# Kernel optimization log

Measured on AMD Instinct MI355X. Metric: run time of the kernel, lower is better.

## Reference

```python
import jax, jax.numpy as jnp
import numpy as np

N, E, F, HID, OUT, B, HEADS = 4096, 131072, 64, 64, 86, 16, 4


def setup_inputs() -> dict:
    key = jax.random.key(0)
    ks = jax.random.split(key, 12)
    s = 0.1
    return {
        "x": jax.random.normal(ks[0], (N, F), dtype=jnp.float32),
        "edge_index": jax.random.randint(ks[1], (2, E), 0, N),
        "edge_attr": jax.random.uniform(ks[2], (E,), dtype=jnp.float32),
        "batch": jnp.sort(jax.random.randint(ks[3], (N,), 0, B)).astype(jnp.int32),
        # GCNConv1: Linear(F -> HID, no bias) + post-aggregation bias
        "W1": jax.random.normal(ks[4], (HID, F), dtype=jnp.float32) * s,
        "b1": jnp.zeros((HID,), jnp.float32),
        # MultiheadAttention(embed_dim=HID, num_heads=4)
        "Win": jax.random.normal(ks[5], (3 * HID, HID), dtype=jnp.float32) * s,
        "b_in": jnp.zeros((3 * HID,), jnp.float32),
        "Wout": jax.random.normal(ks[6], (HID, HID), dtype=jnp.float32) * s,
        "b_out": jnp.zeros((HID,), jnp.float32),
        # GCNConv2: Linear(HID -> OUT)
        "W2": jax.random.normal(ks[7], (OUT, HID), dtype=jnp.float32) * s,
        "b2": jnp.zeros((OUT,), jnp.float32),
    }


def _gcn_layer(h, W, b, src_a, dst_a, norm, n):
    # x' = scatter_add(norm * (x W^T)[src] -> dst) + b   (PyG GCNConv)
    h = h @ W.T
    agg = jax.ops.segment_sum(norm[:, None] * h[src_a], dst_a, num_segments=n)
    return agg + b


def reference(x, edge_index, edge_attr, batch, W1, b1, Win, b_in, Wout, b_out, W2, b2):
    n = x.shape[0]
    # torch.cat([x[:, :-1], x[:, -1:].view(-1,1)], dim=1) == x (identity)
    src, dst = edge_index[0], edge_index[1]
    loop = jnp.arange(n)
    src_a = jnp.concatenate([src, loop])
    dst_a = jnp.concatenate([dst, loop])
    w_a = jnp.concatenate([edge_attr, jnp.ones((n,), x.dtype)])  # self-loops weight 1
    deg = jax.ops.segment_sum(w_a, dst_a, num_segments=n)
    dis = jnp.where(deg > 0, jax.lax.rsqrt(jnp.maximum(deg, 1e-12)), 0.0)
    norm = dis[src_a] * w_a * dis[dst_a]

    h = jax.nn.relu(_gcn_layer(x, W1, b1, src_a, dst_a, norm, n))  # [N, HID]

    # MultiheadAttention over the whole node set as one sequence (batch=1)
    qkv = h @ Win.T + b_in
    q, k, v = jnp.split(qkv, 3, axis=-1)
    dh = HID // HEADS
    to_heads = lambda t: t.reshape(n, HEADS, dh).transpose(1, 0, 2)  # [H, N, dh]
    q, k, v = to_heads(q), to_heads(k), to_heads(v)
    scores = jnp.einsum("hnd,hmd->hnm", q, k) * (1.0 / np.sqrt(dh))
    att = jax.nn.softmax(scores, axis=-1)
    o = jnp.einsum("hnm,hmd->hnd", att, v).transpose(1, 0, 2).reshape(n, HID)
    o = o @ Wout.T + b_out

    h2 = _gcn_layer(o, W2, b2, src_a, dst_a, norm, n)  # [N, OUT]

    # global_mean_pool over graph ids
    sums = jax.ops.segment_sum(h2, batch, num_segments=B)
    cnt = jax.ops.segment_sum(jnp.ones((n,), h2.dtype), batch, num_segments=B)
    return sums / jnp.maximum(cnt, 1.0)[:, None]
```

## Files before the change

### kernel.cpp

```cpp
#include <hip/hip_runtime.h>
#include <hip/hip_bf16.h>

constexpr int N = 4096, E = 131072, OUTF = 86, NB = 16, HEADS = 4, DH = 16;
constexpr int CAP = 128;
constexpr int NSPLIT = 4, KEYS = N / NSPLIT;
constexpr int PCKS = 8;

typedef __attribute__((ext_vector_type(8))) short short8;
typedef __attribute__((ext_vector_type(4))) float f32x4;

constexpr unsigned long long PK_MASK = (1ULL << 40) - 1;
constexpr float PK_SCALE = 1.0f / 16777216.0f;

constexpr size_t OFF_PCK   = 0;
constexpr size_t OFF_INV   = OFF_PCK + 16 * (size_t)N;
constexpr size_t OFF_BUFA  = OFF_INV + 16;
constexpr size_t OFF_QP    = OFF_BUFA + (size_t)N * 64;
constexpr size_t OFF_KP    = OFF_QP + (size_t)N * 32;
constexpr size_t OFF_VP    = OFF_KP + (size_t)N * 32;
constexpr size_t OFF_H2    = OFF_VP + (size_t)N * 32;
constexpr size_t OFF_EPAIR = OFF_H2 + (size_t)N * 86;
constexpr size_t OFF_NORMV = OFF_EPAIR + (size_t)2 * N * CAP;
constexpr size_t OFF_OPART = OFF_NORMV + (size_t)N * CAP;
constexpr size_t OFF_LPART = OFF_OPART + (size_t)HEADS * N * NSPLIT * 16;

__device__ inline unsigned short f2bf(float f) {
    unsigned u = __builtin_bit_cast(unsigned, f);
    u += 0x7FFFu + ((u >> 16) & 1u);
    return (unsigned short)(u >> 16);
}

__device__ inline unsigned pk2bf(float a, float b) {
    __hip_bfloat162 h2 = __float22bfloat162_rn(make_float2(a, b));
    union { __hip_bfloat162 h; unsigned u; } c;
    c.h = h2;
    return c.u;
}

__device__ inline float pk_deg(unsigned long long pk) {
    return (float)(pk & PK_MASK) * PK_SCALE;
}

__global__ __launch_bounds__(256) void d1_kernel(const float* __restrict__ x,
        const float* __restrict__ W1, const int* __restrict__ ei,
        const float* __restrict__ ea, const int* __restrict__ batch,
        const float* __restrict__ b2, float* __restrict__ ws, float* __restrict__ out) {
    __shared__ float4 Ws4[64 * 17];
    __shared__ float4 As4[16 * 17];
    __shared__ int bnd[NB + 1];
    int blk = blockIdx.x, tid = threadIdx.x;
    if (blk < 256) {
        float* bufA = ws + OFF_BUFA;
        for (int idx = tid; idx < 64 * 16; idx += 256)
            Ws4[(idx >> 4) * 17 + (idx & 15)] = ((const float4*)W1)[idx];
        {
            int r = tid >> 4, k4 = tid & 15;
            As4[r * 17 + k4] = ((const float4*)x)[(size_t)(blk * 16 + r) * 16 + k4];
        }
        __syncthreads();
        int r2 = tid & 7, cg = tid >> 3;
        float acc[2][2] = {};
#pragma unroll
        for (int k4 = 0; k4 < 16; ++k4) {
            float4 a0 = As4[r2 * 17 + k4], a1 = As4[(r2 + 8) * 17 + k4];
#pragma unroll
            for (int i = 0; i < 2; ++i) {
                float4 w = Ws4[(cg + 32 * i) * 17 + k4];
                acc[0][i] += a0.x * w.x + a0.y * w.y + a0.z * w.z + a0.w * w.w;
                acc[1][i] += a1.x * w.x + a1.y * w.y + a1.z * w.z + a1.w * w.w;
            }
        }
#pragma unroll
        for (int j = 0; j < 2; ++j)
#pragma unroll
            for (int i = 0; i < 2; ++i)
                bufA[(size_t)(blk * 16 + r2 + 8 * j) * 64 + cg + 32 * i] = acc[j][i];
    } else if (blk < 512) {
        unsigned long long* pck = (unsigned long long*)(ws + OFF_PCK);
        int2* epair = (int2*)(ws + OFF_EPAIR);
        int f = (blk - 256) * 256 + tid;
        int e0 = f, e1 = f + E / 2;
        int s0 = ei[e0], d0 = ei[E + e0];
        int s1 = ei[e1], d1 = ei[E + e1];
        float w0 = ea[e0], w1 = ea[e1];
        unsigned long long a0 = (1ULL << 40) + (unsigned long long)(unsigned)(w0 * 16777216.0f + 0.5f);
        unsigned long long a1 = (1ULL << 40) + (unsigned long long)(unsigned)(w1 * 16777216.0f + 0.5f);
        unsigned long long o0 = atomicAdd(&pck[(size_t)d0 * PCKS], a0);
        unsigned long long o1 = atomicAdd(&pck[(size_t)d1 * PCKS], a1);
        int p0 = (int)(o0 >> 40), p1 = (int)(o1 >> 40);
        if (p0 < CAP) epair[(size_t)d0 * CAP + p0] = make_int2(s0, __float_as_int(w0));
        if (p1 < CAP) epair[(size_t)d1 * CAP + p1] = make_int2(s1, __float_as_int(w1));
    } else {
        float* invcnt = ws + OFF_INV;
        if (tid <= NB) {
            int b = tid, lo = 0, hi = N;
            while (lo < hi) { int m = (lo + hi) >> 1; if (batch[m] < b) lo = m + 1; else hi = m; }
            bnd[tid] = lo;
        }
        __syncthreads();
        if (tid < NB) {
            int cnt = bnd[tid + 1] - bnd[tid];
            invcnt[tid] = cnt > 0 ? 1.0f / (float)cnt : 0.0f;
        }
        for (int idx = tid; idx < NB * OUTF; idx += 256) {
            int b = idx / OUTF;
            int cnt = bnd[b + 1] - bnd[b];
            out[idx] = cnt > 0 ? b2[idx - b * OUTF] : 0.0f;
        }
    }
}

__global__ __launch_bounds__(1024) void d23_kernel(const float* __restrict__ Win,
        const float* __restrict__ b1, const float* __restrict__ b_in,
        float* __restrict__ ws) {
    __shared__ float4 Ws4[16 * 200];
    __shared__ float  Af[16 * 68];

    const unsigned long long* pck = (const unsigned long long*)(ws + OFF_PCK);
    const int2*  epair = (const int2*)(ws + OFF_EPAIR);
    float*       normv = ws + OFF_NORMV;
    const float* bufA  = ws + OFF_BUFA;
    unsigned short* Qp = (unsigned short*)(ws + OFF_QP);
    unsigned short* Kp = (unsigned short*)(ws + OFF_KP);
    unsigned short* Vp = (unsigned short*)(ws + OFF_VP);

    const int tid = threadIdx.x, lane = tid & 63, wv = tid >> 6;
    for (int idx = tid; idx < 192 * 16; idx += 1024) {
        int c = idx >> 4, k4 = idx & 15;
        Ws4[k4 * 200 + c] = ((const float4*)Win)[idx];
    }

    const int node = blockIdx.x * 16 + wv;
    {
        const unsigned long long pkn = pck[(size_t)node * PCKS];
        const float di = rsqrtf(pk_deg(pkn) + 1.0f);
        float acc0 = (di * di) * bufA[(size_t)node * 64 + lane];
        float acc1 = 0.f, acc2 = 0.f, acc3 = 0.f;
        const int cnt = min((int)(pkn >> 40), CAP);
        const int2* pe = epair + (size_t)node * CAP;
        for (int base = 0; base < cnt; base += 64) {
            int rem = cnt - base;
            int   sl = 0;
            float nl = 0.f;
            if (lane < rem) {
                int2 e = pe[base + lane];
                sl = e.x;
                float w = __int_as_float(e.y);
                nl = rsqrtf(pk_deg(pck[(size_t)sl * PCKS]) + 1.0f) * w * di;
                normv[(size_t)node * CAP + base + lane] = nl;
            }
            int m = rem < 64 ? rem : 64;
            int j = 0;
            for (; j + 8 <= m; j += 8) {
                int   s0 = __shfl(sl, j),     s1 = __shfl(sl, j + 1);
                int   s2 = __shfl(sl, j + 2), s3 = __shfl(sl, j + 3);
                int   s4 = __shfl(sl, j + 4), s5 = __shfl(sl, j + 5);
                int   s6 = __shfl(sl, j + 6), s7 = __shfl(sl, j + 7);
                float n0 = __shfl(nl, j),     n1 = __shfl(nl, j + 1);
                float n2 = __shfl(nl, j + 2), n3 = __shfl(nl, j + 3);
                float n4 = __shfl(nl, j + 4), n5 = __shfl(nl, j + 5);
                float n6 = __shfl(nl, j + 6), n7 = __shfl(nl, j + 7);
                float v0 = bufA[(size_t)s0 * 64 + lane], v1 = bufA[(size_t)s1 * 64 + lane];
                float v2 = bufA[(size_t)s2 * 64 + lane], v3 = bufA[(size_t)s3 * 64 + lane];
                float v4 = bufA[(size_t)s4 * 64 + lane], v5 = bufA[(size_t)s5 * 64 + lane];
                float v6 = bufA[(size_t)s6 * 64 + lane], v7 = bufA[(size_t)s7 * 64 + lane];
                acc0 += n0 * v0; acc1 += n1 * v1; acc2 += n2 * v2; acc3 += n3 * v3;
                acc0 += n4 * v4; acc1 += n5 * v5; acc2 += n6 * v6; acc3 += n7 * v7;
            }
            for (; j + 4 <= m; j += 4) {
                int   s0 = __shfl(sl, j),     s1 = __shfl(sl, j + 1);
                int   s2 = __shfl(sl, j + 2), s3 = __shfl(sl, j + 3);
                float n0 = __shfl(nl, j),     n1 = __shfl(nl, j + 1);
                float n2 = __shfl(nl, j + 2), n3 = __shfl(nl, j + 3);
                acc0 += n0 * bufA[(size_t)s0 * 64 + lane];
                acc1 += n1 * bufA[(size_t)s1 * 64 + lane];
                acc2 += n2 * bufA[(size_t)s2 * 64 + lane];
                acc3 += n3 * bufA[(size_t)s3 * 64 + lane];
            }
            for (; j < m; ++j) {
                int   s0 = __shfl(sl, j);
                float n0 = __shfl(nl, j);
                acc0 += n0 * bufA[(size_t)s0 * 64 + lane];
            }
        }
        Af[wv * 68 + lane] = fmaxf((acc0 + acc1) + (acc2 + acc3) + b1[lane], 0.0f);
    }
    __syncthreads();

    {
        const float4* Af4 = (const float4*)Af;
        float acc[3];
#pragma unroll
        for (int i = 0; i < 3; ++i) acc[i] = b_in[lane + 64 * i];
#pragma unroll
        for (int k4 = 0; k4 < 16; ++k4) {
            float4 a = Af4[wv * 17 + k4];
#pragma unroll
            for (int i = 0; i < 3; ++i) {
                float4 w = Ws4[k4 * 200 + lane + 64 * i];
                acc[i] += a.x * w.x + a.y * w.y + a.z * w.z + a.w * w.w;
            }
        }
        const int row = node;
#pragma unroll
        for (int i = 0; i < 3; ++i) {
            int c = lane + 64 * i;
            float v = acc[i];
            if (c < 64) {
                int h = c >> 4, d = c & 15;
                Qp[((size_t)h * N + row) * 16 + d] = f2bf(v * 0.25f);
            } else if (c < 128) {
                int c2 = c - 64, h = c2 >> 4, d = c2 & 15;
                Kp[((size_t)h * N + row) * 16 + d] = f2bf(v);
            } else {
                int c2 = c - 128, h = c2 >> 4, d = c2 & 15;
                Vp[((size_t)h * 16 + d) * N + row] = f2bf(v);
            }
        }
    }
}

__global__ __launch_bounds__(256) void attn_kernel(const float* __restrict__ ws_c,
        float* __restrict__ ws) {
    __shared__ __align__(16) unsigned short Plds[4 * 640];

    const unsigned short* Qp = (const unsigned short*)(ws_c + OFF_QP);
    const unsigned short* Kp = (const unsigned short*)(ws_c + OFF_KP);
    const unsigned short* Vp = (const unsigned short*)(ws_c + OFF_VP);
    float* opart = ws + OFF_OPART;
    float* lpart = ws + OFF_LPART;

    const int h  = blockIdx.y;
    const int sp = blockIdx.z;
    const int k0 = sp * KEYS;
    const int tid = threadIdx.x;
    const int lane = tid & 63, wv = tid >> 6;
    const int q15 = lane & 15, quad = lane >> 4;

    const int qbase = blockIdx.x * 64 + wv * 16;
    short8 qf = {};
    if (quad < 2)
        qf = *(const short8*)&Qp[((size_t)h * N + qbase + q15) * 16 + quad * 8];

    f32x4 O = {0.f, 0.f, 0.f, 0.f};
    float l = 0.f;
    unsigned short* Pw = &Plds[wv * 640];
    const unsigned short* Kh = Kp + (size_t)h * N * 16;
    const unsigned short* Vh = Vp + ((size_t)h * 16 + q15) * N + k0;

#pragma unroll 2
    for (int ch = 0; ch < KEYS / 32; ++ch) {
#pragma unroll
        for (int t = 0; t < 2; ++t) {
            short8 kf = {};
            if (quad < 2)
                kf = *(const short8*)&Kh[(size_t)(k0 + ch * 32 + t * 16 + q15) * 16 + quad * 8];
            f32x4 zero = {0.f, 0.f, 0.f, 0.f};
            __builtin_amdgcn_s_setprio(1);
            f32x4 s = __builtin_amdgcn_mfma_f32_16x16x32_bf16(kf, qf, zero, 0, 0, 0);
            __builtin_amdgcn_s_setprio(0);
            float p0 = __expf(s[0]), p1 = __expf(s[1]), p2 = __expf(s[2]), p3 = __expf(s[3]);
            l += (p0 + p1) + (p2 + p3);
            uint2 pk;
            pk.x = pk2bf(p0, p1);
            pk.y = pk2bf(p2, p3);
            *(uint2*)&Pw[q15 * 40 + t * 16 + quad * 4] = pk;
        }
        asm volatile("s_waitcnt lgkmcnt(0)" ::: "memory");
        short8 pf = *(const short8*)&Pw[q15 * 40 + quad * 8];
        short8 vf = *(const short8*)&Vh[ch * 32 + quad * 8];
        __builtin_amdgcn_s_setprio(1);
        O = __builtin_amdgcn_mfma_f32_16x16x32_bf16(pf, vf, O, 0, 0, 0);
        __builtin_amdgcn_s_setprio(0);
    }

    l += __shfl_xor(l, 16);
    l += __shfl_xor(l, 32);
    if (lane < 16)
        lpart[((size_t)h * N + qbase + q15) * NSPLIT + sp] = l;
#pragma unroll
    for (int r = 0; r < 4; ++r) {
        int query = qbase + quad * 4 + r;
        opart[(((size_t)h * N + query) * NSPLIT + sp) * 16 + q15] = O[r];
    }
}

__global__ __launch_bounds__(256) void d4b_kernel(const float* __restrict__ Wout,
        const float* __restrict__ b_out, const float* __restrict__ W2,
        float* __restrict__ ws) {
    __shared__ float4 WoS[64 * 17];
    __shared__ float4 W2S[96 * 17];
    __shared__ float  o_sh[16 * 68];
    __shared__ float  Bf[16 * 68];

    const float* opart = ws + OFF_OPART;
    const float* lpart = ws + OFF_LPART;
    float* h2pre = ws + OFF_H2;

    const int tid = threadIdx.x, qbase = blockIdx.x * 16;
    for (int idx = tid; idx < 64 * 16; idx += 256)
        WoS[(idx >> 4) * 17 + (idx & 15)] = ((const float4*)Wout)[idx];
    for (int idx = tid; idx < 86 * 16; idx += 256)
        W2S[(idx >> 4) * 17 + (idx & 15)] = ((const float4*)W2)[idx];

    for (int idx = tid; idx < 16 * 64; idx += 256) {
        int r = idx >> 6, f = idx & 63;
        int h = f >> 4, d = f & 15;
        size_t base = ((size_t)h * N + qbase + r) * NSPLIT;
        float L = 0.f, acc = 0.f;
#pragma unroll
        for (int s = 0; s < NSPLIT; ++s) {
            L += lpart[base + s];
            acc += opart[(base + s) * 16 + d];
        }
        o_sh[r * 68 + f] = acc / L;
    }
    __syncthreads();
    {
        int r = tid & 15, c0 = tid >> 4;
        float4* o4 = (float4*)o_sh;
#pragma unroll
        for (int i = 0; i < 4; ++i) {
            int c = c0 + 16 * i;
            float acc = b_out[c];
#pragma unroll
            for (int k4 = 0; k4 < 16; ++k4) {
                float4 a = o4[r * 17 + k4];
                float4 w = WoS[c * 17 + k4];
                acc += a.x * w.x + a.y * w.y + a.z * w.z + a.w * w.w;
            }
            Bf[r * 68 + c] = acc;
        }
    }
    __syncthreads();
    {
        int r = tid & 15, c0 = tid >> 4;
        float4* B4 = (float4*)Bf;
#pragma unroll
        for (int i = 0; i < 6; ++i) {
            int c = c0 + 16 * i;
            if (c < OUTF) {
                float acc = 0.f;
#pragma unroll
                for (int k4 = 0; k4 < 16; ++k4) {
                    float4 a = B4[r * 17 + k4];
                    float4 w = W2S[c * 17 + k4];
                    acc += a.x * w.x + a.y * w.y + a.z * w.z + a.w * w.w;
                }
                h2pre[(size_t)(qbase + r) * OUTF + c] = acc;
            }
        }
    }
}

__global__ __launch_bounds__(1024) void d5_kernel(const int* __restrict__ batch,
        float* __restrict__ ws, float* __restrict__ out) {
    __shared__ float vec[16][88];
    __shared__ int   bix[16];

    const unsigned long long* pck = (const unsigned long long*)(ws + OFF_PCK);
    const int2*  epair = (const int2*)(ws + OFF_EPAIR);
    const float* normv = ws + OFF_NORMV;
    const float* invcnt= ws + OFF_INV;
    const float* h2pre = ws + OFF_H2;

    const int tid = threadIdx.x;
    const int lane = tid & 63, wv = tid >> 6;
    const int node = blockIdx.x * 16 + wv;
    const bool hi2 = lane < (OUTF - 64);
    const int b = batch[node];
    const float inv = invcnt[b];
    const unsigned long long pkn = pck[(size_t)node * PCKS];
    const float di2 = 1.0f / (pk_deg(pkn) + 1.0f);
    const float* Hn = h2pre + (size_t)node * OUTF;
    float a0 = di2 * Hn[lane],                  a1 = 0.f, a2 = 0.f, a3 = 0.f;
    float c0 = hi2 ? di2 * Hn[64 + lane] : 0.f, c1 = 0.f, c2 = 0.f, c3 = 0.f;
    const int cnt = min((int)(pkn >> 40), CAP);
    const int2* pe = epair + (size_t)node * CAP;

    for (int base = 0; base < cnt; base += 64) {
        int rem = cnt - base;
        int   sl = 0;
        float nl = 0.f;
        if (lane < rem) {
            sl = pe[base + lane].x;
            nl = normv[(size_t)node * CAP + base + lane];
        }
        int m = rem < 64 ? rem : 64;
        int j = 0;
        for (; j + 8 <= m; j += 8) {
            int   s0 = __shfl(sl, j),     s1 = __shfl(sl, j + 1);
            int   s2 = __shfl(sl, j + 2), s3 = __shfl(sl, j + 3);
            int   s4 = __shfl(sl, j + 4), s5 = __shfl(sl, j + 5);
            int   s6 = __shfl(sl, j + 6), s7 = __shfl(sl, j + 7);
            float n0 = __shfl(nl, j),     n1 = __shfl(nl, j + 1);
            float n2 = __shfl(nl, j + 2), n3 = __shfl(nl, j + 3);
            float n4 = __shfl(nl, j + 4), n5 = __shfl(nl, j + 5);
            float n6 = __shfl(nl, j + 6), n7 = __shfl(nl, j + 7);
            const float* H0 = h2pre + (size_t)s0 * OUTF;
            const float* H1 = h2pre + (size_t)s1 * OUTF;
            const float* H2 = h2pre + (size_t)s2 * OUTF;
            const float* H3 = h2pre + (size_t)s3 * OUTF;
            const float* H4 = h2pre + (size_t)s4 * OUTF;
            const float* H5 = h2pre + (size_t)s5 * OUTF;
            const float* H6 = h2pre + (size_t)s6 * OUTF;
            const float* H7 = h2pre + (size_t)s7 * OUTF;
            float v0 = H0[lane], v1 = H1[lane], v2 = H2[lane], v3 = H3[lane];
            float v4 = H4[lane], v5 = H5[lane], v6 = H6[lane], v7 = H7[lane];
            a0 += n0 * v0; a1 += n1 * v1; a2 += n2 * v2; a3 += n3 * v3;
            a0 += n4 * v4; a1 += n5 * v5; a2 += n6 * v6; a3 += n7 * v7;
            if (hi2) {
                float w0 = H0[64 + lane], w1 = H1[64 + lane];
                float w2 = H2[64 + lane], w3 = H3[64 + lane];
                float w4 = H4[64 + lane], w5 = H5[64 + lane];
                float w6 = H6[64 + lane], w7 = H7[64 + lane];
                c0 += n0 * w0; c1 += n1 * w1; c2 += n2 * w2; c3 += n3 * w3;
                c0 += n4 * w4; c1 += n5 * w5; c2 += n6 * w6; c3 += n7 * w7;
            }
        }
        for (; j + 4 <= m; j += 4) {
            int   s0 = __shfl(sl, j),     s1 = __shfl(sl, j + 1);
            int   s2 = __shfl(sl, j + 2), s3 = __shfl(sl, j + 3);
            float n0 = __shfl(nl, j),     n1 = __shfl(nl, j + 1);
            float n2 = __shfl(nl, j + 2), n3 = __shfl(nl, j + 3);
            const float* H0 = h2pre + (size_t)s0 * OUTF;
            const float* H1 = h2pre + (size_t)s1 * OUTF;
            const float* H2 = h2pre + (size_t)s2 * OUTF;
            const float* H3 = h2pre + (size_t)s3 * OUTF;
            a0 += n0 * H0[lane]; if (hi2) c0 += n0 * H0[64 + lane];
            a1 += n1 * H1[lane]; if (hi2) c1 += n1 * H1[64 + lane];
            a2 += n2 * H2[lane]; if (hi2) c2 += n2 * H2[64 + lane];
            a3 += n3 * H3[lane]; if (hi2) c3 += n3 * H3[64 + lane];
        }
        for (; j < m; ++j) {
            int   s0 = __shfl(sl, j);
            float n0 = __shfl(nl, j);
            const float* H0 = h2pre + (size_t)s0 * OUTF;
            a0 += n0 * H0[lane];
            if (hi2) c0 += n0 * H0[64 + lane];
        }
    }
    vec[wv][lane] = ((a0 + a1) + (a2 + a3)) * inv;
    if (hi2) vec[wv][64 + lane] = ((c0 + c1) + (c2 + c3)) * inv;
    if (lane == 0) bix[wv] = b;
    __syncthreads();
    if (tid < OUTF) {
        int curb = bix[0];
        float acc = 0.f;
#pragma unroll
        for (int w = 0; w < 16; ++w) {
            int bw = bix[w];
            if (bw != curb) {
                atomicAdd(&out[curb * OUTF + tid], acc);
                curb = bw; acc = 0.f;
            }
            acc += vec[w][tid];
        }
        atomicAdd(&out[curb * OUTF + tid], acc);
    }
}

extern "C" void kernel_launch(void* const* d_in, const int* in_sizes, int n_in,
                              void* d_out, int out_size, void* d_ws, size_t ws_size,
                              hipStream_t stream) {
    const float* x     = (const float*)d_in[0];
    const int*   ei    = (const int*)  d_in[1];
    const float* ea    = (const float*)d_in[2];
    const int*   batch = (const int*)  d_in[3];
    const float* W1    = (const float*)d_in[4];
    const float* b1    = (const float*)d_in[5];
    const float* Win   = (const float*)d_in[6];
    const float* b_in  = (const float*)d_in[7];
    const float* Wout  = (const float*)d_in[8];
    const float* b_out = (const float*)d_in[9];
    const float* W2    = (const float*)d_in[10];
    const float* b2    = (const float*)d_in[11];
    float* out = (float*)d_out;
    float* ws  = (float*)d_ws;

    hipMemsetAsync(ws + OFF_PCK, 0, (size_t)N * 64, stream);
    d1_kernel<<<513, 256, 0, stream>>>(x, W1, ei, ea, batch, b2, ws, out);
    d23_kernel<<<N / 16, 1024, 0, stream>>>(Win, b1, b_in, ws);
    attn_kernel<<<dim3(N / 64, HEADS, NSPLIT), 256, 0, stream>>>(ws, ws);
    d4b_kernel<<<N / 16, 256, 0, stream>>>(Wout, b_out, W2, ws);
    d5_kernel<<<N / 16, 1024, 0, stream>>>(batch, ws, out);
}
```

Measured before the change: 155.0 us.

## Fuse all stages into one cooperative persistent kernel with grid syncs

Replaces five separate kernel launches with a single cooperative kernel of 256 blocks × 1024 threads that runs each stage and uses grid.sync between them. The first stage also merges edge bucketing and the x·W1 projection, each handled by half the waves per block. The aim is to remove launch overhead and inter-kernel gaps. In exchange, the attention and linear stages now run with a fixed 256-block grid and 1024-thread blocks, which can lower occupancy and latency hiding, and each grid.sync adds cost.

```diff
diff --git a/kernel.cpp b/kernel.cpp
--- a/kernel.cpp
+++ b/kernel.cpp
@@ -1,5 +1,8 @@
 #include <hip/hip_runtime.h>
 #include <hip/hip_bf16.h>
+#include <hip/hip_cooperative_groups.h>
+
+namespace cg = cooperative_groups;
 
 constexpr int N = 4096, E = 131072, OUTF = 86, NB = 16, HEADS = 4, DH = 16;
 constexpr int CAP = 128;
@@ -41,57 +44,56 @@
     return (float)(pk & PK_MASK) * PK_SCALE;
 }
 
-__global__ __launch_bounds__(256) void d1_kernel(const float* __restrict__ x,
-        const float* __restrict__ W1, const int* __restrict__ ei,
+__global__ __launch_bounds__(1024) void fused_kernel(
+        const float* __restrict__ x, const int* __restrict__ ei,
         const float* __restrict__ ea, const int* __restrict__ batch,
-        const float* __restrict__ b2, float* __restrict__ ws, float* __restrict__ out) {
-    __shared__ float4 Ws4[64 * 17];
-    __shared__ float4 As4[16 * 17];
-    __shared__ int bnd[NB + 1];
-    int blk = blockIdx.x, tid = threadIdx.x;
-    if (blk < 256) {
-        float* bufA = ws + OFF_BUFA;
-        for (int idx = tid; idx < 64 * 16; idx += 256)
-            Ws4[(idx >> 4) * 17 + (idx & 15)] = ((const float4*)W1)[idx];
-        {
-            int r = tid >> 4, k4 = tid & 15;
-            As4[r * 17 + k4] = ((const float4*)x)[(size_t)(blk * 16 + r) * 16 + k4];
-        }
-        __syncthreads();
-        int r2 = tid & 7, cg = tid >> 3;
-        float acc[2][2] = {};
+        const float* __restrict__ W1, const float* __restrict__ b1,
+        const float* __restrict__ Win, const float* __restrict__ b_in,
+        const float* __restrict__ Wout, const float* __restrict__ b_out,
+        const float* __restrict__ W2, const float* __restrict__ b2,
+        float* __restrict__ ws, float* __restrict__ out) {
+    __shared__ __align__(16) char smem[55552];
+
+    cg::grid_group grid = cg::this_grid();
+
+    const int tid = threadIdx.x, lane = tid & 63, wv = tid >> 6;
+    const int gw = blockIdx.x * 16 + wv;
+
+    unsigned long long* pck = (unsigned long long*)(ws + OFF_PCK);
+    int2*  epair = (int2*)(ws + OFF_EPAIR);
+    float* bufA  = ws + OFF_BUFA;
+    float* invcnt = ws + OFF_INV;
+
+    if (wv < 8) {
+        int e = blockIdx.x * 512 + tid;
+        int s = ei[e], d = ei[E + e];
+        float w = ea[e];
+        unsigned long long a = (1ULL << 40) + (unsigned long long)(unsigned)(w * 16777216.0f + 0.5f);
+        unsigned long long o = atomicAdd(&pck[(size_t)d * PCKS], a);
+        int p = (int)(o >> 40);
+        if (p < CAP) epair[(size_t)d * CAP + p] = make_int2(s, __float_as_int(w));
+    } else {
+        int gw2 = blockIdx.x * 8 + (wv - 8);
+        int r0 = gw2 * 2, r1 = r0 + 1;
+        float4 xa = ((const float4*)x)[(size_t)r0 * 16 + (lane & 15)];
+        float4 xb = ((const float4*)x)[(size_t)r1 * 16 + (lane & 15)];
+        float acc0 = 0.f, acc1 = 0.f;
 #pragma unroll
         for (int k4 = 0; k4 < 16; ++k4) {
-            float4 a0 = As4[r2 * 17 + k4], a1 = As4[(r2 + 8) * 17 + k4];
-#pragma unroll
-            for (int i = 0; i < 2; ++i) {
-                float4 w = Ws4[(cg + 32 * i) * 17 + k4];
-                acc[0][i] += a0.x * w.x + a0.y * w.y + a0.z * w.z + a0.w * w.w;
-                acc[1][i] += a1.x * w.x + a1.y * w.y + a1.z * w.z + a1.w * w.w;
-            }
-        }
-#pragma unroll
-        for (int j = 0; j < 2; ++j)
-#pragma unroll
-            for (int i = 0; i < 2; ++i)
-                bufA[(size_t)(blk * 16 + r2 + 8 * j) * 64 + cg + 32 * i] = acc[j][i];
-    } else if (blk < 512) {
-        unsigned long long* pck = (unsigned long long*)(ws + OFF_PCK);
-        int2* epair = (int2*)(ws + OFF_EPAIR);
-        int f = (blk - 256) * 256 + tid;
-        int e0 = f, e1 = f + E / 2;
-        int s0 = ei[e0], d0 = ei[E + e0];
-        int s1 = ei[e1], d1 = ei[E + e1];
-        float w0 = ea[e0], w1 = ea[e1];
-        unsigned long long a0 = (1ULL << 40) + (unsigned long long)(unsigned)(w0 * 16777216.0f + 0.5f);
-        unsigned long long a1 = (1ULL << 40) + (unsigned long long)(unsigned)(w1 * 16777216.0f + 0.5f);
-        unsigned long long o0 = atomicAdd(&pck[(size_t)d0 * PCKS], a0);
-        unsigned long long o1 = atomicAdd(&pck[(size_t)d1 * PCKS], a1);
-        int p0 = (int)(o0 >> 40), p1 = (int)(o1 >> 40);
-        if (p0 < CAP) epair[(size_t)d0 * CAP + p0] = make_int2(s0, __float_as_int(w0));
-        if (p1 < CAP) epair[(size_t)d1 * CAP + p1] = make_int2(s1, __float_as_int(w1));
-    } else {
-        float* invcnt = ws + OFF_INV;
+            float4 w4 = ((const float4*)W1)[lane * 16 + k4];
+            float ax = __shfl(xa.x, k4), ay = __shfl(xa.y, k4);
+            float az = __shfl(xa.z, k4), aw = __shfl(xa.w, k4);
+            acc0 += ax * w4.x + ay * w4.y + az * w4.z + aw * w4.w;
+            float bx = __shfl(xb.x, k4), by = __shfl(xb.y, k4);
+            float bz = __shfl(xb.z, k4), bw = __shfl(xb.w, k4);
+            acc1 += bx * w4.x + by * w4.y + bz * w4.z + bw * w4.w;
+        }
+        bufA[(size_t)r0 * 64 + lane] = acc0;
+        bufA[(size_t)r1 * 64 + lane] = acc1;
+    }
+    if (blockIdx.x == 0) {
+        int* bnd = (int*)smem;
+        __syncthreads();
         if (tid <= NB) {
             int b = tid, lo = 0, hi = N;
             while (lo < hi) { int m = (lo + hi) >> 1; if (batch[m] < b) lo = m + 1; else hi = m; }
@@ -102,52 +104,275 @@
             int cnt = bnd[tid + 1] - bnd[tid];
             invcnt[tid] = cnt > 0 ? 1.0f / (float)cnt : 0.0f;
         }
-        for (int idx = tid; idx < NB * OUTF; idx += 256) {
+        for (int idx = tid; idx < NB * OUTF; idx += 1024) {
             int b = idx / OUTF;
             int cnt = bnd[b + 1] - bnd[b];
             out[idx] = cnt > 0 ? b2[idx - b * OUTF] : 0.0f;
         }
     }
-}
-
-__global__ __launch_bounds__(1024) void d23_kernel(const float* __restrict__ Win,
-        const float* __restrict__ b1, const float* __restrict__ b_in,
-        float* __restrict__ ws) {
-    __shared__ float4 Ws4[16 * 200];
-    __shared__ float  Af[16 * 68];
-
-    const unsigned long long* pck = (const unsigned long long*)(ws + OFF_PCK);
-    const int2*  epair = (const int2*)(ws + OFF_EPAIR);
-    float*       normv = ws + OFF_NORMV;
-    const float* bufA  = ws + OFF_BUFA;
-    unsigned short* Qp = (unsigned short*)(ws + OFF_QP);
-    unsigned short* Kp = (unsigned short*)(ws + OFF_KP);
-    unsigned short* Vp = (unsigned short*)(ws + OFF_VP);
-
-    const int tid = threadIdx.x, lane = tid & 63, wv = tid >> 6;
-    for (int idx = tid; idx < 192 * 16; idx += 1024) {
-        int c = idx >> 4, k4 = idx & 15;
-        Ws4[k4 * 200 + c] = ((const float4*)Win)[idx];
-    }
-
-    const int node = blockIdx.x * 16 + wv;
+    grid.sync();
+
     {
+        float4* Ws4 = (float4*)smem;
+        float*  Af  = (float*)(smem + 51200);
+        float*       normv = ws + OFF_NORMV;
+        unsigned short* Qp = (unsigned short*)(ws + OFF_QP);
+        unsigned short* Kp = (unsigned short*)(ws + OFF_KP);
+        unsigned short* Vp = (unsigned short*)(ws + OFF_VP);
+
+        for (int idx = tid; idx < 192 * 16; idx += 1024) {
+            int c = idx >> 4, k4 = idx & 15;
+            Ws4[k4 * 200 + c] = ((const float4*)Win)[idx];
+        }
+
+        const int node = gw;
+        {
+            const unsigned long long pkn = pck[(size_t)node * PCKS];
+            const float di = rsqrtf(pk_deg(pkn) + 1.0f);
+            float acc0 = (di * di) * bufA[(size_t)node * 64 + lane];
+            float acc1 = 0.f, acc2 = 0.f, acc3 = 0.f;
+            const int cnt = min((int)(pkn >> 40), CAP);
+            const int2* pe = epair + (size_t)node * CAP;
+            for (int base = 0; base < cnt; base += 64) {
+                int rem = cnt - base;
+                int   sl = 0;
+                float nl = 0.f;
+                if (lane < rem) {
+                    int2 e = pe[base + lane];
+                    sl = e.x;
+                    float w = __int_as_float(e.y);
+                    nl = rsqrtf(pk_deg(pck[(size_t)sl * PCKS]) + 1.0f) * w * di;
+                    normv[(size_t)node * CAP + base + lane] = nl;
+                }
+                int m = rem < 64 ? rem : 64;
+                int j = 0;
+                for (; j + 8 <= m; j += 8) {
+                    int   s0 = __shfl(sl, j),     s1 = __shfl(sl, j + 1);
+                    int   s2 = __shfl(sl, j + 2), s3 = __shfl(sl, j + 3);
+                    int   s4 = __shfl(sl, j + 4), s5 = __shfl(sl, j + 5);
+                    int   s6 = __shfl(sl, j + 6), s7 = __shfl(sl, j + 7);
+                    float n0 = __shfl(nl, j),     n1 = __shfl(nl, j + 1);
+                    float n2 = __shfl(nl, j + 2), n3 = __shfl(nl, j + 3);
+                    float n4 = __shfl(nl, j + 4), n5 = __shfl(nl, j + 5);
+                    float n6 = __shfl(nl, j + 6), n7 = __shfl(nl, j + 7);
+                    float v0 = bufA[(size_t)s0 * 64 + lane], v1 = bufA[(size_t)s1 * 64 + lane];
+                    float v2 = bufA[(size_t)s2 * 64 + lane], v3 = bufA[(size_t)s3 * 64 + lane];
+                    float v4 = bufA[(size_t)s4 * 64 + lane], v5 = bufA[(size_t)s5 * 64 + lane];
+                    float v6 = bufA[(size_t)s6 * 64 + lane], v7 = bufA[(size_t)s7 * 64 + lane];
+                    acc0 += n0 * v0; acc1 += n1 * v1; acc2 += n2 * v2; acc3 += n3 * v3;
+                    acc0 += n4 * v4; acc1 += n5 * v5; acc2 += n6 * v6; acc3 += n7 * v7;
+                }
+                for (; j + 4 <= m; j += 4) {
+                    int   s0 = __shfl(sl, j),     s1 = __shfl(sl, j + 1);
+                    int   s2 = __shfl(sl, j + 2), s3 = __shfl(sl, j + 3);
+                    float n0 = __shfl(nl, j),     n1 = __shfl(nl, j + 1);
+                    float n2 = __shfl(nl, j + 2), n3 = __shfl(nl, j + 3);
+                    acc0 += n0 * bufA[(size_t)s0 * 64 + lane];
+                    acc1 += n1 * bufA[(size_t)s1 * 64 + lane];
+                    acc2 += n2 * bufA[(size_t)s2 * 64 + lane];
+                    acc3 += n3 * bufA[(size_t)s3 * 64 + lane];
+                }
+                for (; j < m; ++j) {
+                    int   s0 = __shfl(sl, j);
+                    float n0 = __shfl(nl, j);
+                    acc0 += n0 * bufA[(size_t)s0 * 64 + lane];
+                }
+            }
+            Af[wv * 68 + lane] = fmaxf((acc0 + acc1) + (acc2 + acc3) + b1[lane], 0.0f);
+        }
+        __syncthreads();
+
+        {
+            const float4* Af4 = (const float4*)Af;
+            float acc[3];
+#pragma unroll
+            for (int i = 0; i < 3; ++i) acc[i] = b_in[lane + 64 * i];
+#pragma unroll
+            for (int k4 = 0; k4 < 16; ++k4) {
+                float4 a = Af4[wv * 17 + k4];
+#pragma unroll
+                for (int i = 0; i < 3; ++i) {
+                    float4 w = Ws4[k4 * 200 + lane + 64 * i];
+                    acc[i] += a.x * w.x + a.y * w.y + a.z * w.z + a.w * w.w;
+                }
+            }
+            const int row = node;
+#pragma unroll
+            for (int i = 0; i < 3; ++i) {
+                int c = lane + 64 * i;
+                float v = acc[i];
+                if (c < 64) {
+                    int h = c >> 4, d = c & 15;
+                    Qp[((size_t)h * N + row) * 16 + d] = f2bf(v * 0.25f);
+                } else if (c < 128) {
+                    int c2 = c - 64, h = c2 >> 4, d = c2 & 15;
+                    Kp[((size_t)h * N + row) * 16 + d] = f2bf(v);
+                } else {
+                    int c2 = c - 128, h = c2 >> 4, d = c2 & 15;
+                    Vp[((size_t)h * 16 + d) * N + row] = f2bf(v);
+                }
+            }
+        }
+    }
+    grid.sync();
+
+    {
+        unsigned short* Plds = (unsigned short*)smem;
+        const unsigned short* Qp = (const unsigned short*)(ws + OFF_QP);
+        const unsigned short* Kp = (const unsigned short*)(ws + OFF_KP);
+        const unsigned short* Vp = (const unsigned short*)(ws + OFF_VP);
+        float* opart = ws + OFF_OPART;
+        float* lpart = ws + OFF_LPART;
+
+        const int qt = gw & 255;
+        const int h  = (gw >> 8) & 3;
+        const int sp = gw >> 10;
+        const int k0 = sp * KEYS;
+        const int q15 = lane & 15, quad = lane >> 4;
+        const int qbase = qt * 16;
+
+        short8 qf = {};
+        if (quad < 2)
+            qf = *(const short8*)&Qp[((size_t)h * N + qbase + q15) * 16 + quad * 8];
+
+        f32x4 O = {0.f, 0.f, 0.f, 0.f};
+        float l = 0.f;
+        unsigned short* Pw = &Plds[wv * 640];
+        const unsigned short* Kh = Kp + (size_t)h * N * 16;
+        const unsigned short* Vh = Vp + ((size_t)h * 16 + q15) * N + k0;
+
+#pragma unroll 2
+        for (int ch = 0; ch < KEYS / 32; ++ch) {
+#pragma unroll
+            for (int t = 0; t < 2; ++t) {
+                short8 kf = {};
+                if (quad < 2)
+                    kf = *(const short8*)&Kh[(size_t)(k0 + ch * 32 + t * 16 + q15) * 16 + quad * 8];
+                f32x4 zero = {0.f, 0.f, 0.f, 0.f};
+                __builtin_amdgcn_s_setprio(1);
+                f32x4 s = __builtin_amdgcn_mfma_f32_16x16x32_bf16(kf, qf, zero, 0, 0, 0);
+                __builtin_amdgcn_s_setprio(0);
+                float p0 = __expf(s[0]), p1 = __expf(s[1]), p2 = __expf(s[2]), p3 = __expf(s[3]);
+                l += (p0 + p1) + (p2 + p3);
+                uint2 pk;
+                pk.x = pk2bf(p0, p1);
+                pk.y = pk2bf(p2, p3);
+                *(uint2*)&Pw[q15 * 40 + t * 16 + quad * 4] = pk;
+            }
+            asm volatile("s_waitcnt lgkmcnt(0)" ::: "memory");
+            short8 pf = *(const short8*)&Pw[q15 * 40 + quad * 8];
+            short8 vf = *(const short8*)&Vh[ch * 32 + quad * 8];
+            __builtin_amdgcn_s_setprio(1);
+            O = __builtin_amdgcn_mfma_f32_16x16x32_bf16(pf, vf, O, 0, 0, 0);
+            __builtin_amdgcn_s_setprio(0);
+        }
+
+        l += __shfl_xor(l, 16);
+        l += __shfl_xor(l, 32);
+        if (lane < 16)
+            lpart[((size_t)h * N + qbase + q15) * NSPLIT + sp] = l;
+#pragma unroll
+        for (int r = 0; r < 4; ++r) {
+            int query = qbase + quad * 4 + r;
+            opart[(((size_t)h * N + query) * NSPLIT + sp) * 16 + q15] = O[r];
+        }
+    }
+    grid.sync();
+
+    {
+        float4* WoS = (float4*)smem;
+        float4* W2S = (float4*)(smem + 17408);
+        float*  o_sh = (float*)(smem + 17408 + 23392);
+        float*  Bf   = (float*)(smem + 17408 + 23392 + 4352);
+
+        const float* opart = ws + OFF_OPART;
+        const float* lpart = ws + OFF_LPART;
+        float* h2pre = ws + OFF_H2;
+        const int qbase = blockIdx.x * 16;
+
+        if (tid < 64 * 16)
+            WoS[(tid >> 4) * 17 + (tid & 15)] = ((const float4*)Wout)[tid];
+        for (int idx = tid; idx < 86 * 16; idx += 1024)
+            W2S[(idx >> 4) * 17 + (idx & 15)] = ((const float4*)W2)[idx];
+
+        {
+            int r = tid >> 6, f = tid & 63;
+            int h = f >> 4, d = f & 15;
+            size_t base = ((size_t)h * N + qbase + r) * NSPLIT;
+            float L = 0.f, acc = 0.f;
+#pragma unroll
+            for (int s = 0; s < NSPLIT; ++s) {
+                L += lpart[base + s];
+                acc += opart[(base + s) * 16 + d];
+            }
+            o_sh[r * 68 + f] = acc / L;
+        }
+        __syncthreads();
+        float bacc;
+        {
+            int r = tid & 15, c = tid >> 4;
+            float4* o4 = (float4*)o_sh;
+            bacc = b_out[c];
+#pragma unroll
+            for (int k4 = 0; k4 < 16; ++k4) {
+                float4 a = o4[r * 17 + k4];
+                float4 w = WoS[c * 17 + k4];
+                bacc += a.x * w.x + a.y * w.y + a.z * w.z + a.w * w.w;
+            }
+        }
+        __syncthreads();
+        {
+            int r = tid & 15, c = tid >> 4;
+            Bf[r * 68 + c] = bacc;
+        }
+        __syncthreads();
+        {
+            int r = tid & 15, c0 = tid >> 4;
+            float4* B4 = (float4*)Bf;
+#pragma unroll
+            for (int i = 0; i < 2; ++i) {
+                int c = c0 + 64 * i;
+                if (c < OUTF) {
+                    float acc = 0.f;
+#pragma unroll
+                    for (int k4 = 0; k4 < 16; ++k4) {
+                        float4 a = B4[r * 17 + k4];
+                        float4 w = W2S[c * 17 + k4];
+                        acc += a.x * w.x + a.y * w.y + a.z * w.z + a.w * w.w;
+                    }
+                    h2pre[(size_t)(qbase + r) * OUTF + c] = acc;
+                }
+            }
+        }
+    }
+    grid.sync();
+
+    {
+        float (*vec)[88] = (float (*)[88])smem;
+        int* bix = (int*)(smem + 5632);
+
+        const float* normv = ws + OFF_NORMV;
+        const float* h2pre = ws + OFF_H2;
+
+        const int node = gw;
+        const bool hi2 = lane < (OUTF - 64);
+        const int b = batch[node];
+        const float inv = invcnt[b];
         const unsigned long long pkn = pck[(size_t)node * PCKS];
-        const float di = rsqrtf(pk_deg(pkn) + 1.0f);
-        float acc0 = (di * di) * bufA[(size_t)node * 64 + lane];
-        float acc1 = 0.f, acc2 = 0.f, acc3 = 0.f;
+        const float di2 = 1.0f / (pk_deg(pkn) + 1.0f);
+        const float* Hn = h2pre + (size_t)node * OUTF;
+        float a0 = di2 * Hn[lane],                  a1 = 0.f, a2 = 0.f, a3 = 0.f;
+        float c0 = hi2 ? di2 * Hn[64 + lane] : 0.f, c1 = 0.f, c2 = 0.f, c3 = 0.f;
         const int cnt = min((int)(pkn >> 40), CAP);
         const int2* pe = epair + (size_t)node * CAP;
+
         for (int base = 0; base < cnt; base += 64) {
             int rem = cnt - base;
             int   sl = 0;
             float nl = 0.f;
             if (lane < rem) {
-                int2 e = pe[base + lane];
-                sl = e.x;
-                float w = __int_as_float(e.y);
-                nl = rsqrtf(pk_deg(pck[(size_t)sl * PCKS]) + 1.0f) * w * di;
-                normv[(size_t)node * CAP + base + lane] = nl;
+                sl = pe[base + lane].x;
+                nl = normv[(size_t)node * CAP + base + lane];
             }
             int m = rem < 64 ? rem : 64;
             int j = 0;
@@ -160,303 +385,67 @@
                 float n2 = __shfl(nl, j + 2), n3 = __shfl(nl, j + 3);
                 float n4 = __shfl(nl, j + 4), n5 = __shfl(nl, j + 5);
                 float n6 = __shfl(nl, j + 6), n7 = __shfl(nl, j + 7);
-                float v0 = bufA[(size_t)s0 * 64 + lane], v1 = bufA[(size_t)s1 * 64 + lane];
-                float v2 = bufA[(size_t)s2 * 64 + lane], v3 = bufA[(size_t)s3 * 64 + lane];
-                float v4 = bufA[(size_t)s4 * 64 + lane], v5 = bufA[(size_t)s5 * 64 + lane];
-                float v6 = bufA[(size_t)s6 * 64 + lane], v7 = bufA[(size_t)s7 * 64 + lane];
-                acc0 += n0 * v0; acc1 += n1 * v1; acc2 += n2 * v2; acc3 += n3 * v3;
-                acc0 += n4 * v4; acc1 += n5 * v5; acc2 += n6 * v6; acc3 += n7 * v7;
+                const float* H0 = h2pre + (size_t)s0 * OUTF;
+                const float* H1 = h2pre + (size_t)s1 * OUTF;
+                const float* H2 = h2pre + (size_t)s2 * OUTF;
+                const float* H3 = h2pre + (size_t)s3 * OUTF;
+                const float* H4 = h2pre + (size_t)s4 * OUTF;
+                const float* H5 = h2pre + (size_t)s5 * OUTF;
+                const float* H6 = h2pre + (size_t)s6 * OUTF;
+                const float* H7 = h2pre + (size_t)s7 * OUTF;
+                float v0 = H0[lane], v1 = H1[lane], v2 = H2[lane], v3 = H3[lane];
+                float v4 = H4[lane], v5 = H5[lane], v6 = H6[lane], v7 = H7[lane];
+                a0 += n0 * v0; a1 += n1 * v1; a2 += n2 * v2; a3 += n3 * v3;
+                a0 += n4 * v4; a1 += n5 * v5; a2 += n6 * v6; a3 += n7 * v7;
+                if (hi2) {
+                    float w0 = H0[64 + lane], w1 = H1[64 + lane];
+                    float w2 = H2[64 + lane], w3 = H3[64 + lane];
+                    float w4 = H4[64 + lane], w5 = H5[64 + lane];
+                    float w6 = H6[64 + lane], w7 = H7[64 + lane];
+                    c0 += n0 * w0; c1 += n1 * w1; c2 += n2 * w2; c3 += n3 * w3;
+                    c0 += n4 * w4; c1 += n5 * w5; c2 += n6 * w6; c3 += n7 * w7;
+                }
             }
             for (; j + 4 <= m; j += 4) {
                 int   s0 = __shfl(sl, j),     s1 = __shfl(sl, j + 1);
                 int   s2 = __shfl(sl, j + 2), s3 = __shfl(sl, j + 3);
                 float n0 = __shfl(nl, j),     n1 = __shfl(nl, j + 1);
                 float n2 = __shfl(nl, j + 2), n3 = __shfl(nl, j + 3);
-                acc0 += n0 * bufA[(size_t)s0 * 64 + lane];
-                acc1 += n1 * bufA[(size_t)s1 * 64 + lane];
-                acc2 += n2 * bufA[(size_t)s2 * 64 + lane];
-                acc3 += n3 * bufA[(size_t)s3 * 64 + lane];
+                const float* H0 = h2pre + (size_t)s0 * OUTF;
+                const float* H1 = h2pre + (size_t)s1 * OUTF;
+                const float* H2 = h2pre + (size_t)s2 * OUTF;
+                const float* H3 = h2pre + (size_t)s3 * OUTF;
+                a0 += n0 * H0[lane]; if (hi2) c0 += n0 * H0[64 + lane];
+                a1 += n1 * H1[lane]; if (hi2) c1 += n1 * H1[64 + lane];
+                a2 += n2 * H2[lane]; if (hi2) c2 += n2 * H2[64 + lane];
+                a3 += n3 * H3[lane]; if (hi2) c3 += n3 * H3[64 + lane];
             }
             for (; j < m; ++j) {
                 int   s0 = __shfl(sl, j);
                 float n0 = __shfl(nl, j);
-                acc0 += n0 * bufA[(size_t)s0 * 64 + lane];
-            }
-        }
-        Af[wv * 68 + lane] = fmaxf((acc0 + acc1) + (acc2 + acc3) + b1[lane], 0.0f);
-    }
-    __syncthreads();
-
-    {
-        const float4* Af4 = (const float4*)Af;
-        float acc[3];
-#pragma unroll
-        for (int i = 0; i < 3; ++i) acc[i] = b_in[lane + 64 * i];
-#pragma unroll
-        for (int k4 = 0; k4 < 16; ++k4) {
-            float4 a = Af4[wv * 17 + k4];
-#pragma unroll
-            for (int i = 0; i < 3; ++i) {
-                float4 w = Ws4[k4 * 200 + lane + 64 * i];
-                acc[i] += a.x * w.x + a.y * w.y + a.z * w.z + a.w * w.w;
-            }
-        }
-        const int row = node;
-#pragma unroll
-        for (int i = 0; i < 3; ++i) {
-            int c = lane + 64 * i;
-            float v = acc[i];
-            if (c < 64) {
-                int h = c >> 4, d = c & 15;
-                Qp[((size_t)h * N + row) * 16 + d] = f2bf(v * 0.25f);
-            } else if (c < 128) {
-                int c2 = c - 64, h = c2 >> 4, d = c2 & 15;
-                Kp[((size_t)h * N + row) * 16 + d] = f2bf(v);
-            } else {
-                int c2 = c - 128, h = c2 >> 4, d = c2 & 15;
-                Vp[((size_t)h * 16 + d) * N + row] = f2bf(v);
-            }
-        }
-    }
-}
-
-__global__ __launch_bounds__(256) void attn_kernel(const float* __restrict__ ws_c,
-        float* __restrict__ ws) {
-    __shared__ __align__(16) unsigned short Plds[4 * 640];
-
-    const unsigned short* Qp = (const unsigned short*)(ws_c + OFF_QP);
-    const unsigned short* Kp = (const unsigned short*)(ws_c + OFF_KP);
-    const unsigned short* Vp = (const unsigned short*)(ws_c + OFF_VP);
-    float* opart = ws + OFF_OPART;
-    float* lpart = ws + OFF_LPART;
-
-    const int h  = blockIdx.y;
-    const int sp = blockIdx.z;
-    const int k0 = sp * KEYS;
-    const int tid = threadIdx.x;
-    const int lane = tid & 63, wv = tid >> 6;
-    const int q15 = lane & 15, quad = lane >> 4;
-
-    const int qbase = blockIdx.x * 64 + wv * 16;
-    short8 qf = {};
-    if (quad < 2)
-        qf = *(const short8*)&Qp[((size_t)h * N + qbase + q15) * 16 + quad * 8];
-
-    f32x4 O = {0.f, 0.f, 0.f, 0.f};
-    float l = 0.f;
-    unsigned short* Pw = &Plds[wv * 640];
-    const unsigned short* Kh = Kp + (size_t)h * N * 16;
-    const unsigned short* Vh = Vp + ((size_t)h * 16 + q15) * N + k0;
-
-#pragma unroll 2
-    for (int ch = 0; ch < KEYS / 32; ++ch) {
-#pragma unroll
-        for (int t = 0; t < 2; ++t) {
-            short8 kf = {};
-            if (quad < 2)
-                kf = *(const short8*)&Kh[(size_t)(k0 + ch * 32 + t * 16 + q15) * 16 + quad * 8];
-            f32x4 zero = {0.f, 0.f, 0.f, 0.f};
-            __builtin_amdgcn_s_setprio(1);
-            f32x4 s = __builtin_amdgcn_mfma_f32_16x16x32_bf16(kf, qf, zero, 0, 0, 0);
-            __builtin_amdgcn_s_setprio(0);
-            float p0 = __expf(s[0]), p1 = __expf(s[1]), p2 = __expf(s[2]), p3 = __expf(s[3]);
-            l += (p0 + p1) + (p2 + p3);
-            uint2 pk;
-            pk.x = pk2bf(p0, p1);
-            pk.y = pk2bf(p2, p3);
-            *(uint2*)&Pw[q15 * 40 + t * 16 + quad * 4] = pk;
-        }
-        asm volatile("s_waitcnt lgkmcnt(0)" ::: "memory");
-        short8 pf = *(const short8*)&Pw[q15 * 40 + quad * 8];
-        short8 vf = *(const short8*)&Vh[ch * 32 + quad * 8];
-        __builtin_amdgcn_s_setprio(1);
-        O = __builtin_amdgcn_mfma_f32_16x16x32_bf16(pf, vf, O, 0, 0, 0);
-        __builtin_amdgcn_s_setprio(0);
-    }
-
-    l += __shfl_xor(l, 16);
-    l += __shfl_xor(l, 32);
-    if (lane < 16)
-        lpart[((size_t)h * N + qbase + q15) * NSPLIT + sp] = l;
-#pragma unroll
-    for (int r = 0; r < 4; ++r) {
-        int query = qbase + quad * 4 + r;
-        opart[(((size_t)h * N + query) * NSPLIT + sp) * 16 + q15] = O[r];
-    }
-}
-
-__global__ __launch_bounds__(256) void d4b_kernel(const float* __restrict__ Wout,
-        const float* __restrict__ b_out, const float* __restrict__ W2,
-        float* __restrict__ ws) {
-    __shared__ float4 WoS[64 * 17];
-    __shared__ float4 W2S[96 * 17];
-    __shared__ float  o_sh[16 * 68];
-    __shared__ float  Bf[16 * 68];
-
-    const float* opart = ws + OFF_OPART;
-    const float* lpart = ws + OFF_LPART;
-    float* h2pre = ws + OFF_H2;
-
-    const int tid = threadIdx.x, qbase = blockIdx.x * 16;
-    for (int idx = tid; idx < 64 * 16; idx += 256)
-        WoS[(idx >> 4) * 17 + (idx & 15)] = ((const float4*)Wout)[idx];
-    for (int idx = tid; idx < 86 * 16; idx += 256)
-        W2S[(idx >> 4) * 17 + (idx & 15)] = ((const float4*)W2)[idx];
-
-    for (int idx = tid; idx < 16 * 64; idx += 256) {
-        int r = idx >> 6, f = idx & 63;
-        int h = f >> 4, d = f & 15;
-        size_t base = ((size_t)h * N + qbase + r) * NSPLIT;
-        float L = 0.f, acc = 0.f;
-#pragma unroll
-        for (int s = 0; s < NSPLIT; ++s) {
-            L += lpart[base + s];
-            acc += opart[(base + s) * 16 + d];
-        }
-        o_sh[r * 68 + f] = acc / L;
-    }
-    __syncthreads();
-    {
-        int r = tid & 15, c0 = tid >> 4;
-        float4* o4 = (float4*)o_sh;
-#pragma unroll
-        for (int i = 0; i < 4; ++i) {
-            int c = c0 + 16 * i;
-            float acc = b_out[c];
-#pragma unroll
-            for (int k4 = 0; k4 < 16; ++k4) {
-                float4 a = o4[r * 17 + k4];
-                float4 w = WoS[c * 17 + k4];
-                acc += a.x * w.x + a.y * w.y + a.z * w.z + a.w * w.w;
-            }
-            Bf[r * 68 + c] = acc;
-        }
-    }
-    __syncthreads();
-    {
-        int r = tid & 15, c0 = tid >> 4;
-        float4* B4 = (float4*)Bf;
-#pragma unroll
-        for (int i = 0; i < 6; ++i) {
-            int c = c0 + 16 * i;
-            if (c < OUTF) {
-                float acc = 0.f;
-#pragma unroll
-                for (int k4 = 0; k4 < 16; ++k4) {
-                    float4 a = B4[r * 17 + k4];
-                    float4 w = W2S[c * 17 + k4];
-                    acc += a.x * w.x + a.y * w.y + a.z * w.z + a.w * w.w;
-                }
-                h2pre[(size_t)(qbase + r) * OUTF + c] = acc;
-            }
-        }
-    }
-}
-
-__global__ __launch_bounds__(1024) void d5_kernel(const int* __restrict__ batch,
-        float* __restrict__ ws, float* __restrict__ out) {
-    __shared__ float vec[16][88];
-    __shared__ int   bix[16];
-
-    const unsigned long long* pck = (const unsigned long long*)(ws + OFF_PCK);
-    const int2*  epair = (const int2*)(ws + OFF_EPAIR);
-    const float* normv = ws + OFF_NORMV;
-    const float* invcnt= ws + OFF_INV;
-    const float* h2pre = ws + OFF_H2;
-
-    const int tid = threadIdx.x;
-    const int lane = tid & 63, wv = tid >> 6;
-    const int node = blockIdx.x * 16 + wv;
-    const bool hi2 = lane < (OUTF - 64);
-    const int b = batch[node];
-    const float inv = invcnt[b];
-    const unsigned long long pkn = pck[(size_t)node * PCKS];
-    const float di2 = 1.0f / (pk_deg(pkn) + 1.0f);
-    const float* Hn = h2pre + (size_t)node * OUTF;
-    float a0 = di2 * Hn[lane],                  a1 = 0.f, a2 = 0.f, a3 = 0.f;
-    float c0 = hi2 ? di2 * Hn[64 + lane] : 0.f, c1 = 0.f, c2 = 0.f, c3 = 0.f;
-    const int cnt = min((int)(pkn >> 40), CAP);
-    const int2* pe = epair + (size_t)node * CAP;
-
-    for (int base = 0; base < cnt; base += 64) {
-        int rem = cnt - base;
-        int   sl = 0;
-        float nl = 0.f;
-        if (lane < rem) {
-            sl = pe[base + lane].x;
-            nl = normv[(size_t)node * CAP + base + lane];
-        }
-        int m = rem < 64 ? rem : 64;
-        int j = 0;
-        for (; j + 8 <= m; j += 8) {
-            int   s0 = __shfl(sl, j),     s1 = __shfl(sl, j + 1);
-            int   s2 = __shfl(sl, j + 2), s3 = __shfl(sl, j + 3);
-            int   s4 = __shfl(sl, j + 4), s5 = __shfl(sl, j + 5);
-            int   s6 = __shfl(sl, j + 6), s7 = __shfl(sl, j + 7);
-            float n0 = __shfl(nl, j),     n1 = __shfl(nl, j + 1);
-            float n2 = __shfl(nl, j + 2), n3 = __shfl(nl, j + 3);
-            float n4 = __shfl(nl, j + 4), n5 = __shfl(nl, j + 5);
-            float n6 = __shfl(nl, j + 6), n7 = __shfl(nl, j + 7);
-            const float* H0 = h2pre + (size_t)s0 * OUTF;
-            const float* H1 = h2pre + (size_t)s1 * OUTF;
-            const float* H2 = h2pre + (size_t)s2 * OUTF;
-            const float* H3 = h2pre + (size_t)s3 * OUTF;
-            const float* H4 = h2pre + (size_t)s4 * OUTF;
-            const float* H5 = h2pre + (size_t)s5 * OUTF;
-            const float* H6 = h2pre + (size_t)s6 * OUTF;
-            const float* H7 = h2pre + (size_t)s7 * OUTF;
-            float v0 = H0[lane], v1 = H1[lane], v2 = H2[lane], v3 = H3[lane];
-            float v4 = H4[lane], v5 = H5[lane], v6 = H6[lane], v7 = H7[lane];
-            a0 += n0 * v0; a1 += n1 * v1; a2 += n2 * v2; a3 += n3 * v3;
-            a0 += n4 * v4; a1 += n5 * v5; a2 += n6 * v6; a3 += n7 * v7;
-            if (hi2) {
-                float w0 = H0[64 + lane], w1 = H1[64 + lane];
-                float w2 = H2[64 + lane], w3 = H3[64 + lane];
-                float w4 = H4[64 + lane], w5 = H5[64 + lane];
-                float w6 = H6[64 + lane], w7 = H7[64 + lane];
-                c0 += n0 * w0; c1 += n1 * w1; c2 += n2 * w2; c3 += n3 * w3;
-                c0 += n4 * w4; c1 += n5 * w5; c2 += n6 * w6; c3 += n7 * w7;
-            }
-        }
-        for (; j + 4 <= m; j += 4) {
-            int   s0 = __shfl(sl, j),     s1 = __shfl(sl, j + 1);
-            int   s2 = __shfl(sl, j + 2), s3 = __shfl(sl, j + 3);
-            float n0 = __shfl(nl, j),     n1 = __shfl(nl, j + 1);
-            float n2 = __shfl(nl, j + 2), n3 = __shfl(nl, j + 3);
-            const float* H0 = h2pre + (size_t)s0 * OUTF;
-            const float* H1 = h2pre + (size_t)s1 * OUTF;
-            const float* H2 = h2pre + (size_t)s2 * OUTF;
-            const float* H3 = h2pre + (size_t)s3 * OUTF;
-            a0 += n0 * H0[lane]; if (hi2) c0 += n0 * H0[64 + lane];
-            a1 += n1 * H1[lane]; if (hi2) c1 += n1 * H1[64 + lane];
-            a2 += n2 * H2[lane]; if (hi2) c2 += n2 * H2[64 + lane];
-            a3 += n3 * H3[lane]; if (hi2) c3 += n3 * H3[64 + lane];
-        }
-        for (; j < m; ++j) {
-            int   s0 = __shfl(sl, j);
-            float n0 = __shfl(nl, j);
-            const float* H0 = h2pre + (size_t)s0 * OUTF;
-            a0 += n0 * H0[lane];
-            if (hi2) c0 += n0 * H0[64 + lane];
-        }
-    }
-    vec[wv][lane] = ((a0 + a1) + (a2 + a3)) * inv;
-    if (hi2) vec[wv][64 + lane] = ((c0 + c1) + (c2 + c3)) * inv;
-    if (lane == 0) bix[wv] = b;
-    __syncthreads();
-    if (tid < OUTF) {
-        int curb = bix[0];
-        float acc = 0.f;
-#pragma unroll
-        for (int w = 0; w < 16; ++w) {
-            int bw = bix[w];
-            if (bw != curb) {
-                atomicAdd(&out[curb * OUTF + tid], acc);
-                curb = bw; acc = 0.f;
-            }
-            acc += vec[w][tid];
-        }
-        atomicAdd(&out[curb * OUTF + tid], acc);
+                const float* H0 = h2pre + (size_t)s0 * OUTF;
+                a0 += n0 * H0[lane];
+                if (hi2) c0 += n0 * H0[64 + lane];
+            }
+        }
+        vec[wv][lane] = ((a0 + a1) + (a2 + a3)) * inv;
+        if (hi2) vec[wv][64 + lane] = ((c0 + c1) + (c2 + c3)) * inv;
+        if (lane == 0) bix[wv] = b;
+        __syncthreads();
+        if (tid < OUTF) {
+            int curb = bix[0];
+            float acc = 0.f;
+#pragma unroll
+            for (int w = 0; w < 16; ++w) {
+                int bw = bix[w];
+                if (bw != curb) {
+                    atomicAdd(&out[curb * OUTF + tid], acc);
+                    curb = bw; acc = 0.f;
+                }
+                acc += vec[w][tid];
+            }
+            atomicAdd(&out[curb * OUTF + tid], acc);
+        }
     }
 }
 
@@ -479,9 +468,9 @@
     float* ws  = (float*)d_ws;
 
     hipMemsetAsync(ws + OFF_PCK, 0, (size_t)N * 64, stream);
-    d1_kernel<<<513, 256, 0, stream>>>(x, W1, ei, ea, batch, b2, ws, out);
-    d23_kernel<<<N / 16, 1024, 0, stream>>>(Win, b1, b_in, ws);
-    attn_kernel<<<dim3(N / 64, HEADS, NSPLIT), 256, 0, stream>>>(ws, ws);
-    d4b_kernel<<<N / 16, 256, 0, stream>>>(Wout, b_out, W2, ws);
-    d5_kernel<<<N / 16, 1024, 0, stream>>>(batch, ws, out);
+
+    void* args[] = {&x, &ei, &ea, &batch, &W1, &b1, &Win, &b_in,
+                    &Wout, &b_out, &W2, &b2, &ws, &out};
+    hipLaunchCooperativeKernel((const void*)fused_kernel, dim3(256), dim3(1024),
+                               args, 0, stream);
 }
```

Result: slower. 295.2 us (+90.5%).
